# Kernel tuning notes

Measured on AMD Instinct MI355X. Metric: run time of the kernel, lower is better.

Reference implementation:

```python
import jax, jax.numpy as jnp
import numpy as np

BATCH, LENGTH, HIDDEN, SSM = 32, 2048, 128, 256


def setup_inputs() -> dict:
    key = jax.random.key(0)
    ks = jax.random.split(key, 7)
    b_std = 1.0 / np.sqrt(HIDDEN)
    c_std = 1.0 / np.sqrt(SSM)
    return {
        "inputs": jax.random.normal(ks[0], (BATCH, LENGTH, HIDDEN), jnp.float32),
        "A_diag": jax.random.normal(ks[1], (SSM,), jnp.float32),
        "G_diag": jax.random.uniform(ks[2], (SSM,), jnp.float32),
        "steps": jax.random.normal(ks[3], (SSM,), jnp.float32) * 0.5,
        "B": jax.random.uniform(ks[4], (SSM, HIDDEN, 2), jnp.float32, -b_std, b_std),
        "C": jax.random.uniform(ks[5], (HIDDEN, SSM, 2), jnp.float32, -c_std, c_std),
        "D": jax.random.normal(ks[6], (HIDDEN,), jnp.float32),
    }


def _project_parameters(A_diag, G_diag, steps):
    # Mirrors DampedLinOSSLayer._project_parameters: sigmoid step, relu damping,
    # and clamp A into the band where the 2x2 IMEX1 transition has complex eigenvalues.
    step = jax.nn.sigmoid(steps)
    g = jax.nn.relu(G_diag)
    denom = jnp.maximum(step * step, 1e-6)
    s = step * g
    base = jnp.sqrt(jnp.maximum(1.0 + s, 1e-6))
    a_low = (2.0 + s - 2.0 * base) / denom
    a_high = (2.0 + s + 2.0 * base) / denom
    a = a_low + jax.nn.relu(A_diag - a_low) - jax.nn.relu(A_diag - a_high)
    return a, g, step


def _eigenvalue(a, g, step):
    # IMEX1 transition M = [[S, -S*dt*A], [dt*S, 1 - dt^2*S*A]] with S = 1/(1+dt*G).
    # det(M) = S, trace(M) = S + 1 - dt^2*S*A; projection guarantees trace^2 < 4*det,
    # so eigenvalues form a conjugate pair lam = T/2 + i*sqrt(S - T^2/4).
    S = 1.0 / (1.0 + step * g)
    T = S + 1.0 - step * step * S * a
    imag = jnp.sqrt(jnp.maximum(S - 0.25 * T * T, 0.0))
    return jax.lax.complex(0.5 * T, imag)  # [P] complex64


def reference(inputs, A_diag, G_diag, steps, B, C, D):
    a, g, step = _project_parameters(A_diag, G_diag, steps)
    lam = _eigenvalue(a, g, step)  # [P]

    # Complex input projection: bu = (B_re + i*B_im) @ u, shape [batch, L, P]
    bu = jax.lax.complex(
        jnp.einsum("blh,ph->blp", inputs, B[..., 0]),
        jnp.einsum("blh,ph->blp", inputs, B[..., 1]),
    )

    # Diagonal complex linear recurrence x_k = lam * x_{k-1} + bu_k via associative scan.
    def combine(e1, e2):
        a1, b1 = e1
        a2, b2 = e2
        return a1 * a2, a2 * b1 + b2

    lam_b = jnp.broadcast_to(lam[None, None, :], bu.shape)
    _, states = jax.lax.associative_scan(combine, (lam_b, bu), axis=1)

    # Output: Re(C @ x) + D * u
    projected = (
        jnp.einsum("blp,hp->blh", states.real, C[..., 0])
        - jnp.einsum("blp,hp->blh", states.imag, C[..., 1])
    )
    return projected + inputs * D
```

## Files before the change

kernel.cpp:

```cpp
#include <hip/hip_runtime.h>
#include <hip/hip_bf16.h>
#include <math.h>

#define BATCH 32
#define LEN   2048
#define HID   128
#define SSM   256

static const size_t PLz = 16777216;
#define BPL 32768
#define CPL 32768

typedef __attribute__((ext_vector_type(4))) float f32x4;
typedef __attribute__((ext_vector_type(8))) short bf16x8;
typedef __attribute__((ext_vector_type(4))) short bf16x4;
typedef __attribute__((ext_vector_type(4))) int   i32x4;
typedef __attribute__((ext_vector_type(2))) unsigned int u32x2;

static __device__ __forceinline__ unsigned short f2bf(float x) {
    union { float f; unsigned u; } v; v.f = x;
    unsigned r = (v.u + 0x7FFFu + ((v.u >> 16) & 1u)) >> 16;
    return (unsigned short)r;
}
static __device__ __forceinline__ unsigned short f2bf_hi(float x) {
    union { float f; unsigned u; } v; v.f = x;
    return (unsigned short)(v.u >> 16);
}
static __device__ __forceinline__ float bf2f(unsigned short b) {
    union { unsigned u; float f; } v; v.u = ((unsigned)b) << 16;
    return v.f;
}
static __device__ __forceinline__ unsigned int cvtpk(float a, float b) {
    __hip_bfloat162 h = __float22bfloat162_rn(float2{a, b});
    union { __hip_bfloat162 h2; unsigned int u; } c; c.h2 = h;
    return c.u;
}
static __device__ __forceinline__ void cmul(float& rr, float& ri,
                                            float ar, float ai, float br, float bi) {
    rr = ar * br - ai * bi;
    ri = ar * bi + ai * br;
}
static __device__ __forceinline__ void gload16(const void* g, void* l) {
    __builtin_amdgcn_global_load_lds(
        (const __attribute__((address_space(1))) unsigned int*)g,
        (__attribute__((address_space(3))) unsigned int*)l,
        16, 0, 0);
}

__global__ __launch_bounds__(256) void k0b_prep(const float* __restrict__ Bm,
                                                const float* __restrict__ Cm,
                                                const float* __restrict__ A,
                                                const float* __restrict__ G,
                                                const float* __restrict__ steps,
                                                unsigned short* __restrict__ Bsp,
                                                unsigned short* __restrict__ Csp,
                                                float* __restrict__ lam) {
    if (blockIdx.x == 256) {
        int p = threadIdx.x;
        if (p < SSM) {
            float stp   = 1.f / (1.f + expf(-steps[p]));
            float g     = fmaxf(G[p], 0.f);
            float denom = fmaxf(stp * stp, 1e-6f);
            float s     = stp * g;
            float base  = sqrtf(fmaxf(1.f + s, 1e-6f));
            float alow  = (2.f + s - 2.f * base) / denom;
            float ahigh = (2.f + s + 2.f * base) / denom;
            float a     = alow + fmaxf(A[p] - alow, 0.f) - fmaxf(A[p] - ahigh, 0.f);
            float S     = 1.f / (1.f + stp * g);
            float T     = S + 1.f - stp * stp * S * a;
            lam[p]       = 0.5f * T;
            lam[SSM + p] = sqrtf(fmaxf(S - 0.25f * T * T, 0.f));
        }
        return;
    }
    int gidx = blockIdx.x * 256 + threadIdx.x;
    if (gidx < 32768) {
        int p = gidx >> 7, h = gidx & 127;
        float vr = Bm[(size_t)(p * HID + h) * 2];
        float vi = Bm[(size_t)(p * HID + h) * 2 + 1];
        unsigned short hh = f2bf_hi(vr);
        Bsp[0 * BPL + p * HID + h] = hh;
        Bsp[1 * BPL + p * HID + h] = f2bf(vr - bf2f(hh));
        hh = f2bf_hi(vi);
        Bsp[2 * BPL + p * HID + h] = hh;
        Bsp[3 * BPL + p * HID + h] = f2bf(vi - bf2f(hh));
    } else {
        int g2 = gidx - 32768;
        int h = g2 >> 8, p = g2 & 255;
        float vr = Cm[(size_t)(h * SSM + p) * 2];
        float vi = -Cm[(size_t)(h * SSM + p) * 2 + 1];
        unsigned short hh = f2bf_hi(vr);
        Csp[0 * CPL + h * SSM + p] = hh;
        Csp[1 * CPL + h * SSM + p] = f2bf(vr - bf2f(hh));
        hh = f2bf_hi(vi);
        Csp[2 * CPL + h * SSM + p] = hh;
        Csp[3 * CPL + h * SSM + p] = f2bf(vi - bf2f(hh));
    }
}

__global__ __launch_bounds__(256) void ku_cvt(const float* __restrict__ u,
                                              unsigned short* __restrict__ ubf) {
    const int total = BATCH * LEN * HID;
    const int stride = 2048 * 256 * 8;
    for (int i = (blockIdx.x * 256 + threadIdx.x) * 8; i < total; i += stride) {
        f32x4 a = *(const f32x4*)&u[i];
        f32x4 c = *(const f32x4*)&u[i + 4];
        i32x4 o;
        o[0] = (int)cvtpk(a[0], a[1]);
        o[1] = (int)cvtpk(a[2], a[3]);
        o[2] = (int)cvtpk(c[0], c[1]);
        o[3] = (int)cvtpk(c[2], c[3]);
        *(i32x4*)&ubf[i] = o;
    }
}

__global__ __launch_bounds__(512, 4) void k12_fused(const unsigned short* __restrict__ ubf,
                                                    const unsigned short* __restrict__ Bsp,
                                                    const float* __restrict__ lam,
                                                    unsigned short* __restrict__ planes) {
    __shared__ __align__(16) char sU[2][32768];
    __shared__ __align__(16) unsigned short sT[2][16][136];
    __shared__ float Rld[4][2][8][2];

    int d    = blockIdx.x;
    int xcd  = d & 7;
    int idx  = d >> 3;
    int pt   = idx & 15;
    int bhi  = idx >> 4;
    int b    = bhi * 8 + xcd;
    int p0   = pt * 16;

    int tid  = threadIdx.x;
    int lane = tid & 63, w = tid >> 6;
    int wl   = w >> 1, wp = w & 1;
    int fr   = lane & 15, g = lane >> 4;
    int frp  = fr & 7;
    int comp = fr >> 3;
    int pcol = p0 + wp * 8 + frp;

    const unsigned short* Bh  = Bsp + (size_t)(comp * 2) * BPL + (size_t)pcol * HID;
    const unsigned short* Blo = Bsp + (size_t)(comp * 2 + 1) * BPL + (size_t)pcol * HID;
    bf16x8 Bfh[4], Bfl[4];
#pragma unroll
    for (int kc = 0; kc < 4; ++kc) {
        Bfh[kc] = *(const bf16x8*)&Bh[kc * 32 + g * 8];
        Bfl[kc] = *(const bf16x8*)&Blo[kc * 32 + g * 8];
    }

    float pw_r[4], pw_i[4];
    float lg_r, lg_i;
    float l4r, l4i, l8r, l8i, l16r, l16i, l32r, l32i;
    {
        float ar = lam[pcol], ai = lam[SSM + pcol];
        pw_r[0] = ar; pw_i[0] = ai;
        cmul(pw_r[1], pw_i[1], ar, ai, ar, ai);
        cmul(pw_r[2], pw_i[2], pw_r[1], pw_i[1], ar, ai);
        cmul(pw_r[3], pw_i[3], pw_r[1], pw_i[1], pw_r[1], pw_i[1]);
        l4r = pw_r[3]; l4i = pw_i[3];
        cmul(l8r, l8i, l4r, l4i, l4r, l4i);
        cmul(l16r, l16i, l8r, l8i, l8r, l8i);
        cmul(l32r, l32i, l16r, l16i, l16r, l16i);
        if (g == 0)      { lg_r = 1.f; lg_i = 0.f; }
        else if (g == 1) { lg_r = l4r; lg_i = l4i; }
        else if (g == 2) { lg_r = l8r; lg_i = l8i; }
        else             { cmul(lg_r, lg_i, l8r, l8i, l4r, l4i); }
    }

    float TCr = 0.f, TCi = 0.f;

    const unsigned short* ub = ubf + (size_t)b * (LEN * HID);
    int srow32  = tid >> 4;
    int stg_src = srow32 * HID + ((((tid & 15) * 16) ^ ((srow32 & 7) << 4)) >> 1);

#define STAGE(buf, tt)                                                        \
    {                                                                         \
        const unsigned short* gs = ub + (size_t)(tt) * 16384 + stg_src;       \
        char* ls = &sU[buf][tid * 16];                                        \
        _Pragma("unroll")                                                     \
        for (int q = 0; q < 4; ++q)                                           \
            gload16(gs + q * 4096, ls + q * 8192);                            \
    }

    STAGE(0, 0)
    __syncthreads();
    int cur = 0;

    for (int t = 0; t < 16; ++t) {
        int l0t = t * 128;

        if (t < 15) STAGE(cur ^ 1, t + 1)

        const char* su = &sU[cur][0];
        f32x4 acc[2];
        acc[0] = (f32x4)(0.f); acc[1] = (f32x4)(0.f);
#pragma unroll
        for (int kc = 0; kc < 4; ++kc) {
#pragma unroll
            for (int mi = 0; mi < 2; ++mi) {
                int off = (wl * 32 + mi * 16 + fr) * 256 + ((kc * 64 + g * 16) ^ ((fr & 7) << 4));
                bf16x8 ah = *(const bf16x8*)(su + off);
                acc[mi] = __builtin_amdgcn_mfma_f32_16x16x32_bf16(ah, Bfh[kc], acc[mi], 0, 0, 0);
                acc[mi] = __builtin_amdgcn_mfma_f32_16x16x32_bf16(ah, Bfl[kc], acc[mi], 0, 0, 0);
            }
        }

        float xr[4], xi[4];
#pragma unroll
        for (int e = 0; e < 4; ++e) {
            float send = (comp == 0) ? acc[1][e] : acc[0][e];
            float oth  = __shfl_xor(send, 8, 64);
            xr[e] = (comp == 0) ? acc[0][e] : oth;
            xi[e] = (comp == 0) ? oth       : acc[1][e];
        }

        float Er, Ei, Fr, Fi, For, Foi;
        {
            float lr = pw_r[0], li = pw_i[0];
            float cr = 0.f, ci = 0.f;
#pragma unroll
            for (int r = 0; r < 4; ++r) {
                float nr = fmaf(lr, cr, fmaf(-li, ci, xr[r]));
                float ni = fmaf(lr, ci, fmaf(li, cr, xi[r]));
                cr = nr; ci = ni;
                xr[r] = cr; xi[r] = ci;
            }
            float Qr = cr, Qi = ci;
            float ur = __shfl_up(Qr, 16u, 64);
            float ui = __shfl_up(Qi, 16u, 64);
            if (g >= 1) {
                Qr = fmaf(l4r, ur, fmaf(-l4i, ui, Qr));
                Qi = fmaf(l4r, ui, fmaf(l4i, ur, Qi));
            }
            ur = __shfl_up(Qr, 32u, 64);
            ui = __shfl_up(Qi, 32u, 64);
            if (g >= 2) {
                Qr = fmaf(l8r, ur, fmaf(-l8i, ui, Qr));
                Qi = fmaf(l8r, ui, fmaf(l8i, ur, Qi));
            }
            Er = __shfl_up(Qr, 16u, 64);
            Ei = __shfl_up(Qi, 16u, 64);
            if (g == 0) { Er = 0.f; Ei = 0.f; }
            Fr = __shfl(Qr, fr + 48, 64);
            Fi = __shfl(Qi, fr + 48, 64);
            For = __shfl_xor(Fr, 8, 64);
            Foi = __shfl_xor(Fi, 8, 64);
            float Rr = fmaf(l16r, For, fmaf(-l16i, Foi, Fr));
            float Ri = fmaf(l16r, Foi, fmaf(l16i, For, Fi));
            if (g == 0 && fr >= 8) { Rld[wl][wp][frp][0] = Rr; Rld[wl][wp][frp][1] = Ri; }
        }
        __syncthreads();

        {
            float Wr = TCr, Wi = TCi;
            float Tr = TCr, Ti = TCi;
#pragma unroll
            for (int w2 = 0; w2 < 4; ++w2) {
                float rr = Rld[w2][wp][frp][0], ri = Rld[w2][wp][frp][1];
                float nTr = fmaf(l32r, Tr, fmaf(-l32i, Ti, rr));
                float nTi = fmaf(l32r, Ti, fmaf(l32i, Tr, ri));
                Tr = nTr; Ti = nTi;
                if (w2 < wl) {
                    float nWr = fmaf(l32r, Wr, fmaf(-l32i, Wi, rr));
                    float nWi = fmaf(l32r, Wi, fmaf(l32i, Wr, ri));
                    Wr = nWr; Wi = nWi;
                }
            }
            TCr = Tr; TCi = Ti;
            float prr, pri;
            if (comp == 0) { prr = Wr; pri = Wi; }
            else {
                prr = fmaf(l16r, Wr, fmaf(-l16i, Wi, For));
                pri = fmaf(l16r, Wi, fmaf(l16i, Wr, Foi));
            }
            float Mr = fmaf(lg_r, prr, fmaf(-lg_i, pri, Er));
            float Mi = fmaf(lg_r, pri, fmaf(lg_i, prr, Ei));
#pragma unroll
            for (int r = 0; r < 4; ++r) {
                xr[r] = fmaf(pw_r[r], Mr, fmaf(-pw_i[r], Mi, xr[r]));
                xi[r] = fmaf(pw_r[r], Mi, fmaf(pw_i[r], Mr, xi[r]));
            }
        }

        {
            int col = wl * 32 + comp * 16 + g * 4;
            u32x2 pk0, pk1;
            pk0.x = cvtpk(xr[0], xr[1]); pk0.y = cvtpk(xr[2], xr[3]);
            pk1.x = cvtpk(xi[0], xi[1]); pk1.y = cvtpk(xi[2], xi[3]);
            *(u32x2*)&sT[0][wp * 8 + frp][col] = pk0;
            *(u32x2*)&sT[1][wp * 8 + frp][col] = pk1;
        }
        __syncthreads();

        {
            int rowid = tid >> 4;
            int pl = rowid >> 4, pp = rowid & 15;
            int c8 = (tid & 15) * 8;
            bf16x8 v = *(const bf16x8*)&sT[pl][pp][c8];
            *(bf16x8*)&planes[(size_t)pl * PLz +
                    ((size_t)(b * SSM + p0 + pp)) * LEN + l0t + c8] = v;
        }
        cur ^= 1;
    }
#undef STAGE
}

__global__ __launch_bounds__(256) void k3_out(const unsigned short* __restrict__ planes,
                                              const unsigned short* __restrict__ Csp,
                                              const unsigned short* __restrict__ ubf,
                                              const float* __restrict__ D,
                                              float* __restrict__ out) {
    __shared__ __align__(16) unsigned short sA[2][128][40];
    __shared__ __align__(16) unsigned short sC[4][128][40];
    int d   = blockIdx.x;
    int xcd = d & 7;
    int grp = d >> 3;
    int lt  = grp & 15;
    int bhi = grp >> 4;
    int b   = bhi * 8 + xcd;
    int l0  = lt * 128;

    int tid = threadIdx.x;
    int lane = tid & 63, w = tid >> 6;
    int wl = w >> 1, wh = w & 1;
    int fr = lane & 15, g = lane >> 4;

    f32x4 acc[4][4];
#pragma unroll
    for (int mi = 0; mi < 4; ++mi)
#pragma unroll
        for (int ni = 0; ni < 4; ++ni) acc[mi][ni] = (f32x4)(0.f);

    float dv[4];
#pragma unroll
    for (int ni = 0; ni < 4; ++ni) dv[ni] = D[wh * 64 + ni * 16 + fr];

    for (int pc = 0; pc < SSM; pc += 32) {
        {
            int loct = tid & 15;
#pragma unroll
            for (int r = 0; r < 2; ++r) {
                int p_ = (tid >> 4) + 16 * r;
                int rot = (loct + p_) & 7;
#pragma unroll
                for (int pl = 0; pl < 2; ++pl) {
                    union { bf16x8 v; unsigned long long q[2]; } U;
                    U.v = *(const bf16x8*)&planes[(size_t)pl * PLz +
                            ((size_t)(b * SSM + pc + p_)) * LEN + l0 + loct * 8];
                    unsigned long long x0 = U.q[0], x1 = U.q[1];
                    if (rot & 4) { unsigned long long tq = x0; x0 = x1; x1 = tq; }
                    if (rot & 2) {
                        unsigned long long n0 = (x0 >> 32) | (x1 << 32);
                        unsigned long long n1 = (x1 >> 32) | (x0 << 32);
                        x0 = n0; x1 = n1;
                    }
                    if (rot & 1) {
                        unsigned long long n0 = (x0 >> 16) | (x1 << 48);
                        unsigned long long n1 = (x1 >> 16) | (x0 << 48);
                        x0 = n0; x1 = n1;
                    }
                    int rb = loct * 8;
                    sA[pl][rb + ((0 + rot) & 7)][p_] = (unsigned short)(x0);
                    sA[pl][rb + ((1 + rot) & 7)][p_] = (unsigned short)(x0 >> 16);
                    sA[pl][rb + ((2 + rot) & 7)][p_] = (unsigned short)(x0 >> 32);
                    sA[pl][rb + ((3 + rot) & 7)][p_] = (unsigned short)(x0 >> 48);
                    sA[pl][rb + ((4 + rot) & 7)][p_] = (unsigned short)(x1);
                    sA[pl][rb + ((5 + rot) & 7)][p_] = (unsigned short)(x1 >> 16);
                    sA[pl][rb + ((6 + rot) & 7)][p_] = (unsigned short)(x1 >> 32);
                    sA[pl][rb + ((7 + rot) & 7)][p_] = (unsigned short)(x1 >> 48);
                }
            }
        }
        {
            int poct = tid & 3;
#pragma unroll
            for (int r2 = 0; r2 < 2; ++r2) {
                int hh = (tid >> 2) + 64 * r2;
#pragma unroll
                for (int pl = 0; pl < 4; ++pl) {
                    i32x4 v = *(const i32x4*)&Csp[(size_t)pl * CPL + (size_t)hh * SSM + pc + poct * 8];
                    *(i32x4*)&sC[pl][hh][poct * 8] = v;
                }
            }
        }
        __syncthreads();

        int kk = g * 8;
        bf16x8 crh[4], crl[4], cih[4], cil[4];
#pragma unroll
        for (int ni = 0; ni < 4; ++ni) {
            int hr = wh * 64 + ni * 16 + fr;
            crh[ni] = *(const bf16x8*)&sC[0][hr][kk];
            crl[ni] = *(const bf16x8*)&sC[1][hr][kk];
            cih[ni] = *(const bf16x8*)&sC[2][hr][kk];
            cil[ni] = *(const bf16x8*)&sC[3][hr][kk];
        }
#pragma unroll
        for (int mi = 0; mi < 4; ++mi) {
            int lr_ = wl * 64 + mi * 16 + fr;
            bf16x8 ar = *(const bf16x8*)&sA[0][lr_][kk];
            bf16x8 ai = *(const bf16x8*)&sA[1][lr_][kk];
#pragma unroll
            for (int ni = 0; ni < 4; ++ni) {
                acc[mi][ni] = __builtin_amdgcn_mfma_f32_16x16x32_bf16(ar, crh[ni], acc[mi][ni], 0, 0, 0);
                acc[mi][ni] = __builtin_amdgcn_mfma_f32_16x16x32_bf16(ar, crl[ni], acc[mi][ni], 0, 0, 0);
                acc[mi][ni] = __builtin_amdgcn_mfma_f32_16x16x32_bf16(ai, cih[ni], acc[mi][ni], 0, 0, 0);
                acc[mi][ni] = __builtin_amdgcn_mfma_f32_16x16x32_bf16(ai, cil[ni], acc[mi][ni], 0, 0, 0);
            }
        }
        __syncthreads();
    }

#pragma unroll
    for (int mi = 0; mi < 4; ++mi)
#pragma unroll
        for (int ni = 0; ni < 4; ++ni) {
            int lb = l0 + wl * 64 + mi * 16 + g * 4;
            int h = wh * 64 + ni * 16 + fr;
#pragma unroll
            for (int r = 0; r < 4; ++r) {
                size_t idx = ((size_t)b * LEN + lb + r) * HID + h;
                out[idx] = acc[mi][ni][r] + bf2f(ubf[idx]) * dv[ni];
            }
        }
}

extern "C" void kernel_launch(void* const* d_in, const int* in_sizes, int n_in,
                              void* d_out, int out_size, void* d_ws, size_t ws_size,
                              hipStream_t stream) {
    const float* u  = (const float*)d_in[0];
    const float* A  = (const float*)d_in[1];
    const float* G  = (const float*)d_in[2];
    const float* st = (const float*)d_in[3];
    const float* B  = (const float*)d_in[4];
    const float* C  = (const float*)d_in[5];
    const float* D  = (const float*)d_in[6];
    float* out = (float*)d_out;

    char* WS = (char*)d_ws;
    unsigned short* planes = (unsigned short*)WS;
    float* lam             = (float*)(WS + 67108864);
    unsigned short* Bsp    = (unsigned short*)(WS + 67110912);
    unsigned short* Csp    = (unsigned short*)(WS + 67373056);
    unsigned short* ubf    = (unsigned short*)(WS + 67635200);

    k0b_prep<<<257, 256, 0, stream>>>(B, C, A, G, st, Bsp, Csp, lam);
    ku_cvt<<<2048, 256, 0, stream>>>(u, ubf);
    k12_fused<<<512, 512, 0, stream>>>(ubf, Bsp, lam, planes);
    k3_out<<<512, 256, 0, stream>>>(planes, Csp, ubf, D, out);
}
```

Baseline: 90.69 us.

## Store scan states row-major interleaved and pipeline output GEMM with async LDS loads

The scan kernel now writes states as interleaved re/im bf16 pairs in an [l][p] row-major layout with an XOR-swizzled LDS transpose. The separate real and imaginary planes are gone. The output GEMM interleaves the C hi/lo splits the same way, so each k-step needs half as many MFMAs per operand load. It also replaces the scalar transposing LDS scatter with double-buffered global_load_lds and swizzled reads, and splits the hidden dimension across twice as many blocks. This is meant to remove the costly shuffle-transpose and uncoalesced traffic in k3, at the cost of a different state layout and more grid launches.

```diff
diff --git a/kernel.cpp b/kernel.cpp
--- a/kernel.cpp
+++ b/kernel.cpp
@@ -7,15 +7,11 @@
 #define HID   128
 #define SSM   256
 
-static const size_t PLz = 16777216;
 #define BPL 32768
-#define CPL 32768
 
 typedef __attribute__((ext_vector_type(4))) float f32x4;
 typedef __attribute__((ext_vector_type(8))) short bf16x8;
-typedef __attribute__((ext_vector_type(4))) short bf16x4;
 typedef __attribute__((ext_vector_type(4))) int   i32x4;
-typedef __attribute__((ext_vector_type(2))) unsigned int u32x2;
 
 static __device__ __forceinline__ unsigned short f2bf(float x) {
     union { float f; unsigned u; } v; v.f = x;
@@ -53,7 +49,7 @@
                                                 const float* __restrict__ G,
                                                 const float* __restrict__ steps,
                                                 unsigned short* __restrict__ Bsp,
-                                                unsigned short* __restrict__ Csp,
+                                                unsigned short* __restrict__ C2,
                                                 float* __restrict__ lam) {
     if (blockIdx.x == 256) {
         int p = threadIdx.x;
@@ -89,12 +85,13 @@
         int h = g2 >> 8, p = g2 & 255;
         float vr = Cm[(size_t)(h * SSM + p) * 2];
         float vi = -Cm[(size_t)(h * SSM + p) * 2 + 1];
-        unsigned short hh = f2bf_hi(vr);
-        Csp[0 * CPL + h * SSM + p] = hh;
-        Csp[1 * CPL + h * SSM + p] = f2bf(vr - bf2f(hh));
-        hh = f2bf_hi(vi);
-        Csp[2 * CPL + h * SSM + p] = hh;
-        Csp[3 * CPL + h * SSM + p] = f2bf(vi - bf2f(hh));
+        unsigned short rh = f2bf_hi(vr);
+        unsigned short ih = f2bf_hi(vi);
+        size_t rowh = (size_t)h * 512;
+        C2[rowh + 2 * p]               = rh;
+        C2[rowh + 2 * p + 1]           = ih;
+        C2[65536 + rowh + 2 * p]       = f2bf(vr - bf2f(rh));
+        C2[65536 + rowh + 2 * p + 1]   = f2bf(vi - bf2f(ih));
     }
 }
 
@@ -117,9 +114,9 @@
 __global__ __launch_bounds__(512, 4) void k12_fused(const unsigned short* __restrict__ ubf,
                                                     const unsigned short* __restrict__ Bsp,
                                                     const float* __restrict__ lam,
-                                                    unsigned short* __restrict__ planes) {
+                                                    unsigned short* __restrict__ TP) {
     __shared__ __align__(16) char sU[2][32768];
-    __shared__ __align__(16) unsigned short sT[2][16][136];
+    __shared__ __align__(16) char sT2[10240];
     __shared__ float Rld[4][2][8][2];
 
     int d    = blockIdx.x;
@@ -282,140 +279,118 @@
         }
 
         {
-            int col = wl * 32 + comp * 16 + g * 4;
-            u32x2 pk0, pk1;
-            pk0.x = cvtpk(xr[0], xr[1]); pk0.y = cvtpk(xr[2], xr[3]);
-            pk1.x = cvtpk(xi[0], xi[1]); pk1.y = cvtpk(xi[2], xi[3]);
-            *(u32x2*)&sT[0][wp * 8 + frp][col] = pk0;
-            *(u32x2*)&sT[1][wp * 8 + frp][col] = pk1;
+            int colb  = wl * 32 + comp * 16 + g * 4;
+            int idxu  = wp * 8 + frp;
+            int piece = idxu >> 2, sub = idxu & 3;
+            int pw    = piece ^ g;
+#pragma unroll
+            for (int r = 0; r < 4; ++r) {
+                unsigned int pk = cvtpk(xr[r], xi[r]);
+                *(unsigned int*)(sT2 + (colb + r) * 80 + pw * 16 + sub * 4) = pk;
+            }
         }
         __syncthreads();
 
         {
-            int rowid = tid >> 4;
-            int pl = rowid >> 4, pp = rowid & 15;
-            int c8 = (tid & 15) * 8;
-            bf16x8 v = *(const bf16x8*)&sT[pl][pp][c8];
-            *(bf16x8*)&planes[(size_t)pl * PLz +
-                    ((size_t)(b * SSM + p0 + pp)) * LEN + l0t + c8] = v;
+            int row = tid >> 2, q = tid & 3;
+            int x2  = (row >> 2) & 3;
+            bf16x8 v = *(const bf16x8*)(sT2 + row * 80 + ((q ^ x2) * 16));
+            *(bf16x8*)&TP[((size_t)(b * LEN) + l0t + row) * 512 + p0 * 2 + q * 8] = v;
         }
         cur ^= 1;
     }
 #undef STAGE
 }
 
-__global__ __launch_bounds__(256) void k3_out(const unsigned short* __restrict__ planes,
-                                              const unsigned short* __restrict__ Csp,
-                                              const unsigned short* __restrict__ ubf,
-                                              const float* __restrict__ D,
-                                              float* __restrict__ out) {
-    __shared__ __align__(16) unsigned short sA[2][128][40];
-    __shared__ __align__(16) unsigned short sC[4][128][40];
-    int d   = blockIdx.x;
-    int xcd = d & 7;
-    int grp = d >> 3;
-    int lt  = grp & 15;
-    int bhi = grp >> 4;
-    int b   = bhi * 8 + xcd;
-    int l0  = lt * 128;
+__global__ __launch_bounds__(256, 4) void k3_out(const unsigned short* __restrict__ TP,
+                                                 const unsigned short* __restrict__ C2,
+                                                 const unsigned short* __restrict__ ubf,
+                                                 const float* __restrict__ D,
+                                                 float* __restrict__ out) {
+    __shared__ __align__(16) char sAB[2][16384];
+
+    int d    = blockIdx.x;
+    int xcd  = d & 7;
+    int rest = d >> 3;
+    int ht   = rest & 1;
+    int lt   = (rest >> 1) & 15;
+    int bhi  = rest >> 5;
+    int b    = bhi * 8 + xcd;
+    int l0   = lt * 128;
+    int h0   = ht * 64;
 
     int tid = threadIdx.x;
     int lane = tid & 63, w = tid >> 6;
     int wl = w >> 1, wh = w & 1;
     int fr = lane & 15, g = lane >> 4;
 
-    f32x4 acc[4][4];
+    f32x4 acc[4][2];
 #pragma unroll
     for (int mi = 0; mi < 4; ++mi)
 #pragma unroll
-        for (int ni = 0; ni < 4; ++ni) acc[mi][ni] = (f32x4)(0.f);
-
-    float dv[4];
-#pragma unroll
-    for (int ni = 0; ni < 4; ++ni) dv[ni] = D[wh * 64 + ni * 16 + fr];
-
-    for (int pc = 0; pc < SSM; pc += 32) {
-        {
-            int loct = tid & 15;
-#pragma unroll
-            for (int r = 0; r < 2; ++r) {
-                int p_ = (tid >> 4) + 16 * r;
-                int rot = (loct + p_) & 7;
-#pragma unroll
-                for (int pl = 0; pl < 2; ++pl) {
-                    union { bf16x8 v; unsigned long long q[2]; } U;
-                    U.v = *(const bf16x8*)&planes[(size_t)pl * PLz +
-                            ((size_t)(b * SSM + pc + p_)) * LEN + l0 + loct * 8];
-                    unsigned long long x0 = U.q[0], x1 = U.q[1];
-                    if (rot & 4) { unsigned long long tq = x0; x0 = x1; x1 = tq; }
-                    if (rot & 2) {
-                        unsigned long long n0 = (x0 >> 32) | (x1 << 32);
-                        unsigned long long n1 = (x1 >> 32) | (x0 << 32);
-                        x0 = n0; x1 = n1;
-                    }
-                    if (rot & 1) {
-                        unsigned long long n0 = (x0 >> 16) | (x1 << 48);
-                        unsigned long long n1 = (x1 >> 16) | (x0 << 48);
-                        x0 = n0; x1 = n1;
-                    }
-                    int rb = loct * 8;
-                    sA[pl][rb + ((0 + rot) & 7)][p_] = (unsigned short)(x0);
-                    sA[pl][rb + ((1 + rot) & 7)][p_] = (unsigned short)(x0 >> 16);
-                    sA[pl][rb + ((2 + rot) & 7)][p_] = (unsigned short)(x0 >> 32);
-                    sA[pl][rb + ((3 + rot) & 7)][p_] = (unsigned short)(x0 >> 48);
-                    sA[pl][rb + ((4 + rot) & 7)][p_] = (unsigned short)(x1);
-                    sA[pl][rb + ((5 + rot) & 7)][p_] = (unsigned short)(x1 >> 16);
-                    sA[pl][rb + ((6 + rot) & 7)][p_] = (unsigned short)(x1 >> 32);
-                    sA[pl][rb + ((7 + rot) & 7)][p_] = (unsigned short)(x1 >> 48);
-                }
-            }
-        }
-        {
-            int poct = tid & 3;
-#pragma unroll
-            for (int r2 = 0; r2 < 2; ++r2) {
-                int hh = (tid >> 2) + 64 * r2;
-#pragma unroll
-                for (int pl = 0; pl < 4; ++pl) {
-                    i32x4 v = *(const i32x4*)&Csp[(size_t)pl * CPL + (size_t)hh * SSM + pc + poct * 8];
-                    *(i32x4*)&sC[pl][hh][poct * 8] = v;
-                }
+        for (int ni = 0; ni < 2; ++ni) acc[mi][ni] = (f32x4)(0.f);
+
+    float dv[2];
+#pragma unroll
+    for (int ni = 0; ni < 2; ++ni) dv[ni] = D[h0 + wh * 32 + ni * 16 + fr];
+
+#define STAGE3(buf, cc)                                                       \
+    {                                                                         \
+        _Pragma("unroll")                                                     \
+        for (int q = 0; q < 2; ++q) {                                         \
+            int dg = tid + q * 256; int rw = dg >> 2, sl = dg & 3;            \
+            gload16(TP + ((size_t)(b * LEN) + l0 + rw) * 512 + (cc) * 32 +    \
+                        ((sl ^ (rw & 3)) * 8),                                \
+                    &sAB[buf][dg * 16]);                                      \
+        }                                                                     \
+        _Pragma("unroll")                                                     \
+        for (int q = 0; q < 2; ++q) {                                         \
+            int dg = tid + q * 256; int hl = dg >> 8, hr = (dg >> 2) & 63;    \
+            int sl = dg & 3;                                                  \
+            gload16(C2 + ((size_t)(hl * 128 + h0 + hr)) * 512 + (cc) * 32 +   \
+                        ((sl ^ (hr & 3)) * 8),                                \
+                    &sAB[buf][8192 + dg * 16]);                               \
+        }                                                                     \
+    }
+
+    STAGE3(0, 0)
+    __syncthreads();
+    int cur = 0;
+
+    for (int c = 0; c < 16; ++c) {
+        if (c < 15) STAGE3(cur ^ 1, c + 1)
+
+        const char* sb = &sAB[cur][0];
+        int swz = (g ^ (fr & 3)) * 16;
+        bf16x8 bfr[2][2];
+#pragma unroll
+        for (int ni = 0; ni < 2; ++ni) {
+            int hrow = wh * 32 + ni * 16 + fr;
+#pragma unroll
+            for (int hl = 0; hl < 2; ++hl)
+                bfr[ni][hl] = *(const bf16x8*)(sb + 8192 + hl * 4096 + hrow * 64 + swz);
+        }
+#pragma unroll
+        for (int mi = 0; mi < 4; ++mi) {
+            int arow = wl * 64 + mi * 16 + fr;
+            bf16x8 af = *(const bf16x8*)(sb + arow * 64 + swz);
+#pragma unroll
+            for (int ni = 0; ni < 2; ++ni) {
+                acc[mi][ni] = __builtin_amdgcn_mfma_f32_16x16x32_bf16(af, bfr[ni][0], acc[mi][ni], 0, 0, 0);
+                acc[mi][ni] = __builtin_amdgcn_mfma_f32_16x16x32_bf16(af, bfr[ni][1], acc[mi][ni], 0, 0, 0);
             }
         }
         __syncthreads();
-
-        int kk = g * 8;
-        bf16x8 crh[4], crl[4], cih[4], cil[4];
-#pragma unroll
-        for (int ni = 0; ni < 4; ++ni) {
-            int hr = wh * 64 + ni * 16 + fr;
-            crh[ni] = *(const bf16x8*)&sC[0][hr][kk];
-            crl[ni] = *(const bf16x8*)&sC[1][hr][kk];
-            cih[ni] = *(const bf16x8*)&sC[2][hr][kk];
-            cil[ni] = *(const bf16x8*)&sC[3][hr][kk];
-        }
-#pragma unroll
-        for (int mi = 0; mi < 4; ++mi) {
-            int lr_ = wl * 64 + mi * 16 + fr;
-            bf16x8 ar = *(const bf16x8*)&sA[0][lr_][kk];
-            bf16x8 ai = *(const bf16x8*)&sA[1][lr_][kk];
-#pragma unroll
-            for (int ni = 0; ni < 4; ++ni) {
-                acc[mi][ni] = __builtin_amdgcn_mfma_f32_16x16x32_bf16(ar, crh[ni], acc[mi][ni], 0, 0, 0);
-                acc[mi][ni] = __builtin_amdgcn_mfma_f32_16x16x32_bf16(ar, crl[ni], acc[mi][ni], 0, 0, 0);
-                acc[mi][ni] = __builtin_amdgcn_mfma_f32_16x16x32_bf16(ai, cih[ni], acc[mi][ni], 0, 0, 0);
-                acc[mi][ni] = __builtin_amdgcn_mfma_f32_16x16x32_bf16(ai, cil[ni], acc[mi][ni], 0, 0, 0);
-            }
-        }
-        __syncthreads();
-    }
+        cur ^= 1;
+    }
+#undef STAGE3
 
 #pragma unroll
     for (int mi = 0; mi < 4; ++mi)
 #pragma unroll
-        for (int ni = 0; ni < 4; ++ni) {
+        for (int ni = 0; ni < 2; ++ni) {
             int lb = l0 + wl * 64 + mi * 16 + g * 4;
-            int h = wh * 64 + ni * 16 + fr;
+            int h  = h0 + wh * 32 + ni * 16 + fr;
 #pragma unroll
             for (int r = 0; r < 4; ++r) {
                 size_t idx = ((size_t)b * LEN + lb + r) * HID + h;
@@ -437,14 +412,14 @@
     float* out = (float*)d_out;
 
     char* WS = (char*)d_ws;
-    unsigned short* planes = (unsigned short*)WS;
-    float* lam             = (float*)(WS + 67108864);
-    unsigned short* Bsp    = (unsigned short*)(WS + 67110912);
-    unsigned short* Csp    = (unsigned short*)(WS + 67373056);
-    unsigned short* ubf    = (unsigned short*)(WS + 67635200);
-
-    k0b_prep<<<257, 256, 0, stream>>>(B, C, A, G, st, Bsp, Csp, lam);
+    unsigned short* TP  = (unsigned short*)WS;
+    float* lam          = (float*)(WS + 67108864);
+    unsigned short* Bsp = (unsigned short*)(WS + 67110912);
+    unsigned short* C2  = (unsigned short*)(WS + 67373056);
+    unsigned short* ubf = (unsigned short*)(WS + 67635200);
+
+    k0b_prep<<<257, 256, 0, stream>>>(B, C, A, G, st, Bsp, C2, lam);
     ku_cvt<<<2048, 256, 0, stream>>>(u, ubf);
-    k12_fused<<<512, 512, 0, stream>>>(ubf, Bsp, lam, planes);
-    k3_out<<<512, 256, 0, stream>>>(planes, Csp, ubf, D, out);
-}
+    k12_fused<<<512, 512, 0, stream>>>(ubf, Bsp, lam, TP);
+    k3_out<<<1024, 256, 0, stream>>>(TP, C2, ubf, D, out);
+}
```

Result: no change. 90.84 us (+0.2%).
